# Kernel tuning notes

Hardware: AMD Instinct MI355X
Metric: run time of the kernel (lower is better)

The kernel has to match this reference:

```python
import jax, jax.numpy as jnp
import numpy as np

EPS = 1e-5

def rmsnorm(x, w):
    var = jnp.mean(x * x, axis=-1, keepdims=True)
    return x * jax.lax.rsqrt(var + EPS) * w


def setup_inputs() -> dict:
    key = jax.random.key(0)
    B, L, dim = 4, 2048, 1024
    d_inner, d_state, d_conv, dt_rank = 2 * dim, 16, 4, dim // 16
    ks = jax.random.split(key, 8)
    g = lambda k, shape, scale: (jax.random.normal(k, shape, jnp.float32) * scale)
    return {
        "x": g(ks[0], (B, L, dim), 1.0),
        "rms_w": jnp.ones((dim,), jnp.float32),
        "in_proj": g(ks[1], (dim, 2 * d_inner), dim ** -0.5),
        "conv_w": g(ks[2], (d_inner, d_conv), 0.25),
        "conv_b": jnp.zeros((d_inner,), jnp.float32),
        "x_proj": g(ks[3], (d_inner, dt_rank + 2 * d_state), d_inner ** -0.5),
        "dt_w": g(ks[4], (dt_rank, d_inner), dt_rank ** -0.5),
        # inverse-softplus(0.01): softplus(dt_b) ~ 0.01 at init, standard Mamba dt init
        "dt_b": jnp.full((d_inner,), float(np.log(np.expm1(0.01))), jnp.float32),
        # S4D-real init: A_n = -(n+1)
        "A_log": jnp.log(jnp.broadcast_to(jnp.arange(1, d_state + 1, dtype=jnp.float32), (d_inner, d_state))).copy(),
        "D": jnp.ones((d_inner,), jnp.float32),
        "out_proj": g(ks[5], (d_inner, dim), d_inner ** -0.5),
    }


def _mamba_block(x, rms_w, in_proj, conv_w, conv_b, x_proj, dt_w, dt_b, A_log, D, out_proj):
    B, L, dim = x.shape
    d_inner, K = conv_w.shape
    d_state = A_log.shape[1]
    dt_rank = dt_w.shape[0]

    xn = rmsnorm(x, rms_w)
    xz = xn @ in_proj                      # [B,L,2*d_inner]
    xi, z = jnp.split(xz, 2, axis=-1)

    # causal depthwise conv1d over L
    xc = jax.lax.conv_general_dilated(
        xi.transpose(0, 2, 1),             # [B,C,L]
        conv_w[:, None, :],                # [C,1,K]
        window_strides=(1,), padding=[(K - 1, 0)],
        feature_group_count=d_inner,
    ).transpose(0, 2, 1) + conv_b
    xi = jax.nn.silu(xc)                   # [B,L,d_inner]

    dbc = xi @ x_proj                      # [B,L,dt_rank+2*d_state]
    dt, Bm, Cm = jnp.split(dbc, [dt_rank, dt_rank + d_state], axis=-1)
    delta = jax.nn.softplus(dt @ dt_w + dt_b)  # [B,L,d_inner]
    A = -jnp.exp(A_log)                    # [d_inner,d_state]

    def step(h, inputs):
        d_t, x_t, B_t, C_t = inputs        # [B,d_inner],[B,d_inner],[B,d_state],[B,d_state]
        dA = jnp.exp(d_t[..., None] * A)   # [B,d_inner,d_state]
        h = dA * h + (d_t * x_t)[..., None] * B_t[:, None, :]
        y = jnp.einsum('bds,bs->bd', h, C_t)
        return h, y

    h0 = jnp.zeros((B, d_inner, d_state), x.dtype)
    xs = (delta.transpose(1, 0, 2), xi.transpose(1, 0, 2),
          Bm.transpose(1, 0, 2), Cm.transpose(1, 0, 2))
    _, ys = jax.lax.scan(step, h0, xs)     # ys: [L,B,d_inner]

    y = ys.transpose(1, 0, 2) + xi * D     # D skip connection
    y = y * jax.nn.silu(z)                 # output gate
    return x + y @ out_proj                # residual


def reference(x, rms_w, in_proj, conv_w, conv_b, x_proj, dt_w, dt_b, A_log, D, out_proj):
    return _mamba_block(x, rms_w, in_proj, conv_w, conv_b, x_proj, dt_w, dt_b, A_log, D, out_proj)
```

## Files before the change

kernel.cpp:

```cpp
#include <hip/hip_runtime.h>
#include <hip/hip_bf16.h>
#include <math.h>


#define ROWS 8192
#define DIM 1024
#define DINNER 2048
#define DSTATE 16
#define DTRANK 64
#define LSEQ 2048
#define NCHUNK 32
#define LCHUNK 64

#define LOG2E 1.4426950408889634f

typedef unsigned short ushort;
typedef __attribute__((ext_vector_type(8))) short short8;
typedef __attribute__((ext_vector_type(4))) float float4v;

__device__ inline ushort f2bf(float f) {
    __hip_bfloat16 h = __float2bfloat16(f);
    return *reinterpret_cast<ushort*>(&h);
}
__device__ inline float bf2f(ushort u) {
    union { unsigned int i; float f; } w; w.i = ((unsigned int)u) << 16; return w.f;
}

__device__ inline float fexp2(float x) {
#if __has_builtin(__builtin_amdgcn_exp2f)
    return __builtin_amdgcn_exp2f(x);
#else
    return __expf(x * 0.69314718056f);
#endif
}

__device__ inline void dma16(const void* g, void* l) {
    __builtin_amdgcn_global_load_lds(
        (const __attribute__((address_space(1))) unsigned int*)g,
        (__attribute__((address_space(3))) unsigned int*)l, 16, 0, 0);
}

template <int N> __device__ inline void vwait() {
    if constexpr (N == 0)      asm volatile("s_waitcnt vmcnt(0)" ::: "memory");
    else if constexpr (N == 3) asm volatile("s_waitcnt vmcnt(3)" ::: "memory");
    else if constexpr (N == 4) asm volatile("s_waitcnt vmcnt(4)" ::: "memory");
    else if constexpr (N == 6) asm volatile("s_waitcnt vmcnt(6)" ::: "memory");
    else static_assert(N < 0, "unsupported vmcnt literal");
}

__global__ __launch_bounds__(256)
void prep_kernel(const float* __restrict__ in_proj, ushort* __restrict__ bt1,
                 const float* __restrict__ out_proj, ushort* __restrict__ bt2,
                 const float* __restrict__ x_proj, ushort* __restrict__ bt3,
                 const float* __restrict__ dt_w, ushort* __restrict__ bt4,
                 const float* __restrict__ x, const float* __restrict__ rms_w,
                 ushort* __restrict__ xn) {
    __shared__ float tld[32][33];
    __shared__ float red[4];
    int bid = blockIdx.x, tid = threadIdx.x;
    if (bid < 6464) {
        const float* in; ushort* outT; int R, C, bx, by;
        if (bid < 4096)      { in = in_proj;  outT = bt1; R = 1024; C = 4096; bx = bid & 127; by = bid >> 7; }
        else if (bid < 6144) { int t = bid - 4096; in = out_proj; outT = bt2; R = 2048; C = 1024; bx = t & 31; by = t >> 5; }
        else if (bid < 6336) { int t = bid - 6144; in = x_proj;  outT = bt3; R = 2048; C = 96;  bx = t % 3;  by = t / 3; }
        else                 { int t = bid - 6336; in = dt_w;    outT = bt4; R = 64;   C = 2048; bx = t & 63; by = t >> 6; }
        int tx = tid & 31, ty = tid >> 5;
#pragma unroll
        for (int k = 0; k < 4; ++k)
            tld[ty + k * 8][tx] = in[(long)(by * 32 + ty + k * 8) * C + bx * 32 + tx];
        __syncthreads();
#pragma unroll
        for (int k = 0; k < 4; ++k)
            outT[(long)(bx * 32 + ty + k * 8) * R + by * 32 + tx] = f2bf(tld[tx][ty + k * 8]);
    } else {
        int row = bid - 6464;
        float4 xv = ((const float4*)(x + (long)row * DIM))[tid];
        float ss = xv.x * xv.x + xv.y * xv.y + xv.z * xv.z + xv.w * xv.w;
        for (int off = 32; off > 0; off >>= 1) ss += __shfl_down(ss, off);
        if ((tid & 63) == 0) red[tid >> 6] = ss;
        __syncthreads();
        float scale = rsqrtf((red[0] + red[1] + red[2] + red[3]) / DIM + 1e-5f);
        float4 wv = ((const float4*)rms_w)[tid];
        ushort4 ov;
        ov.x = f2bf(xv.x * scale * wv.x);
        ov.y = f2bf(xv.y * scale * wv.y);
        ov.z = f2bf(xv.z * scale * wv.z);
        ov.w = f2bf(xv.w * scale * wv.w);
        ((ushort4*)xn)[(long)row * 256 + tid] = ov;
    }
}

template <int MW, int NW, int MF, int NF, int EPI>
__global__ __launch_bounds__(MW * NW * 64, 4)
void gemm_ring(const ushort* __restrict__ A, int lda,
               const ushort* __restrict__ Bt, int ldbt,
               void* __restrict__ Cv, int ldc, int K,
               const float* __restrict__ aux) {
    constexpr int W    = MW * NW;
    constexpr int BLKM = MW * MF * 16;
    constexpr int BLKN = NW * NF * 16;
    constexpr int TILE = (BLKM + BLKN) * 32;
    constexpr int NA   = BLKM / (16 * W);
    constexpr int NB   = BLKN / (16 * W);
    __shared__ __align__(16) ushort lds[2 * TILE];

    const int tid  = threadIdx.x;
    const int w    = tid >> 6, lane = tid & 63;
    const int wm   = w / NW,   wn   = w % NW;
    const int quad = lane >> 4, l16 = lane & 15;
    const long row0 = (long)blockIdx.y * BLKM;
    const long col0 = (long)blockIdx.x * BLKN;

    const ushort* gA[NA];
    const ushort* gB[NB];
#pragma unroll
    for (int i = 0; i < NA; ++i)
        gA[i] = A + (row0 + (w + i * W) * 16 + l16) * lda + quad * 8;
#pragma unroll
    for (int i = 0; i < NB; ++i)
        gB[i] = Bt + (col0 + (w + i * W) * 16 + l16) * ldbt + quad * 8;

    const int NT = K >> 5;
    float4v acc[MF][NF] = {};

    auto stage = [&](int kt, int slot) {
        ushort* lb = lds + slot * TILE;
        const int ko = kt << 5;
#pragma unroll
        for (int i = 0; i < NA; ++i)
            dma16(gA[i] + ko, lb + (w + i * W) * 512);
#pragma unroll
        for (int i = 0; i < NB; ++i)
            dma16(gB[i] + ko, lb + BLKM * 32 + (w + i * W) * 512);
    };

    stage(0, 0);
    vwait<0>();
    __builtin_amdgcn_s_barrier();

    for (int t = 0; t < NT; ++t) {
        const int s = t & 1;
        if (t + 1 < NT) stage(t + 1, s ^ 1);
        const ushort* lb  = lds + s * TILE;
        const ushort* lbB = lb + BLKM * 32;
        short8 af[MF], bfr[NF];
#pragma unroll
        for (int m = 0; m < MF; ++m)
            af[m] = *reinterpret_cast<const short8*>(
                &lb[(wm * MF + m) * 512 + lane * 8]);
#pragma unroll
        for (int n = 0; n < NF; ++n)
            bfr[n] = *reinterpret_cast<const short8*>(
                &lbB[(wn * NF + n) * 512 + lane * 8]);
        __builtin_amdgcn_s_setprio(1);
#pragma unroll
        for (int m = 0; m < MF; ++m)
#pragma unroll
            for (int n = 0; n < NF; ++n)
                acc[m][n] = __builtin_amdgcn_mfma_f32_16x16x32_bf16(
                    af[m], bfr[n], acc[m][n], 0, 0, 0);
        __builtin_amdgcn_s_setprio(0);
        vwait<0>();
        if (t < NT - 1) __builtin_amdgcn_s_barrier();
    }

#pragma unroll
    for (int m = 0; m < MF; ++m) {
#pragma unroll
        for (int n = 0; n < NF; ++n) {
            long rbase = row0 + wm * (MF * 16) + m * 16 + quad * 4;
            long c = col0 + wn * (NF * 16) + n * 16 + l16;
#pragma unroll
            for (int r = 0; r < 4; ++r) {
                float v = acc[m][n][r];
                long idx = (rbase + r) * (long)ldc + c;
                if (EPI == 2) ((float*)Cv)[idx] = v + aux[idx];
                else          ((ushort*)Cv)[idx] = f2bf(v);
            }
        }
    }
}

__global__ __launch_bounds__(256)
void xproj_conv_gemm(const ushort* __restrict__ xz,
                     const float* __restrict__ cw, const float* __restrict__ cb,
                     const ushort* __restrict__ bt3,
                     float* __restrict__ dbcp) {
    __shared__ __align__(16) ushort As[128][32];
    __shared__ __align__(16) ushort Bs[128][32];
    int tid = threadIdx.x;
    int wave = tid >> 6, lane = tid & 63;
    int wm = wave >> 1, wn = wave & 1;
    int quad = lane >> 4, l16 = lane & 15;
    int row0 = blockIdx.y * 128;
    int ks0 = blockIdx.x * 512;
    int srow = tid >> 2, sseg = tid & 3;

    int r0 = (wave * 2 + 0) * 16 + (lane >> 2);
    int r1 = (wave * 2 + 1) * 16 + (lane >> 2);
    int ksl = (lane & 3) * 8;
    const ushort* b0 = bt3 + (long)r0 * 2048 + ks0 + ksl;
    const ushort* b1 = bt3 + (long)r1 * 2048 + ks0 + ksl;
    ushort* lB0 = &Bs[(wave * 2 + 0) * 16][0];
    ushort* lB1 = &Bs[(wave * 2 + 1) * 16][0];

    float4v acc[4][4] = {};

    for (int k0 = 0; k0 < 512; k0 += 32) {
        dma16(b0 + k0, lB0);
        dma16(b1 + k0, lB1);
#pragma unroll
        for (int it = 0; it < 2; ++it) {
            int r = srow + it * 64;
            long row = row0 + r;
            int l = (int)(row & (LSEQ - 1));
            int cch = ks0 + k0 + sseg * 8;
            short8 v[4];
#pragma unroll
            for (int t = 0; t < 4; ++t) {
                if (l - 3 + t >= 0) v[t] = *(const short8*)&xz[(row - 3 + t) * 4096 + cch];
                else { short8 zz = {0,0,0,0,0,0,0,0}; v[t] = zz; }
            }
            ushort o[8];
#pragma unroll
            for (int j = 0; j < 8; ++j) {
                float4 w = ((const float4*)cw)[cch + j];
                float a = cb[cch + j]
                        + bf2f((ushort)v[0][j]) * w.x + bf2f((ushort)v[1][j]) * w.y
                        + bf2f((ushort)v[2][j]) * w.z + bf2f((ushort)v[3][j]) * w.w;
                a = a / (1.f + __expf(-a));
                o[j] = f2bf(a);
            }
            *(short8*)&As[r][sseg * 8] = *(const short8*)o;
        }
        __syncthreads();

        short8 afrag[4], bfrag[4];
#pragma unroll
        for (int i = 0; i < 4; ++i)
            afrag[i] = *reinterpret_cast<const short8*>(&As[wm * 64 + i * 16 + l16][quad * 8]);
#pragma unroll
        for (int j = 0; j < 4; ++j)
            bfrag[j] = *reinterpret_cast<const short8*>(&Bs[wn * 64 + j * 16 + l16][quad * 8]);
#pragma unroll
        for (int i = 0; i < 4; ++i)
#pragma unroll
            for (int j = 0; j < 4; ++j)
                acc[i][j] = __builtin_amdgcn_mfma_f32_16x16x32_bf16(
                    afrag[i], bfrag[j], acc[i][j], 0, 0, 0);
        __syncthreads();
    }
    float* dst = dbcp + (long)blockIdx.x * ROWS * 96;
#pragma unroll
    for (int i = 0; i < 4; ++i) {
#pragma unroll
        for (int j = 0; j < 4; ++j) {
            int rbase = row0 + wm * 64 + i * 16 + quad * 4;
            int c = wn * 64 + j * 16 + l16;
            if (c < 96) {
#pragma unroll
                for (int r = 0; r < 4; ++r)
                    dst[(long)(rbase + r) * 96 + c] = acc[i][j][r];
            }
        }
    }
}

__global__ __launch_bounds__(256)
void dbc_reduce(const float4* __restrict__ dbcp, float4* __restrict__ dbc) {
    int i = blockIdx.x * 256 + threadIdx.x;
    float4 a = dbcp[i];
    float4 b = dbcp[i + 196608];
    float4 c = dbcp[i + 2 * 196608];
    float4 d = dbcp[i + 3 * 196608];
    float4 o;
    o.x = a.x + b.x + c.x + d.x;
    o.y = a.y + b.y + c.y + d.y;
    o.z = a.z + b.z + c.z + d.z;
    o.w = a.w + b.w + c.w + d.w;
    dbc[i] = o;
}

__global__ __launch_bounds__(256)
void mfma_gemm_dt(const float* __restrict__ A, int lda,
                  const ushort* __restrict__ Bt, int ldbt,
                  ushort* __restrict__ C, int ldc, int K,
                  const float* __restrict__ aux) {
    __shared__ __align__(16) ushort As[128][40];
    __shared__ __align__(16) ushort Bs[128][40];
    int tid = threadIdx.x;
    int wave = tid >> 6, lane = tid & 63;
    int wm = wave >> 1, wn = wave & 1;
    int quad = lane >> 4, l16 = lane & 15;
    int row0 = blockIdx.y * 128, col0 = blockIdx.x * 128;
    int srow = tid >> 2, sseg = tid & 3;

    float4v acc[4][4] = {};

    for (int k0 = 0; k0 < K; k0 += 32) {
#pragma unroll
        for (int it = 0; it < 2; ++it) {
            int r = srow + it * 64;
            const float* ap = A + (long)(row0 + r) * lda + k0 + sseg * 8;
            ushort tmp[8];
#pragma unroll
            for (int j = 0; j < 8; ++j) tmp[j] = f2bf(ap[j]);
            *reinterpret_cast<short8*>(&As[r][sseg * 8]) =
                *reinterpret_cast<const short8*>(tmp);
            const ushort* bp = Bt + (long)(col0 + r) * ldbt + k0 + sseg * 8;
            *reinterpret_cast<short8*>(&Bs[r][sseg * 8]) =
                *reinterpret_cast<const short8*>(bp);
        }
        __syncthreads();
        short8 afrag[4], bfrag[4];
#pragma unroll
        for (int i = 0; i < 4; ++i)
            afrag[i] = *reinterpret_cast<const short8*>(&As[wm * 64 + i * 16 + l16][quad * 8]);
#pragma unroll
        for (int j = 0; j < 4; ++j)
            bfrag[j] = *reinterpret_cast<const short8*>(&Bs[wn * 64 + j * 16 + l16][quad * 8]);
#pragma unroll
        for (int i = 0; i < 4; ++i)
#pragma unroll
            for (int j = 0; j < 4; ++j)
                acc[i][j] = __builtin_amdgcn_mfma_f32_16x16x32_bf16(
                    afrag[i], bfrag[j], acc[i][j], 0, 0, 0);
        __syncthreads();
    }
#pragma unroll
    for (int i = 0; i < 4; ++i) {
#pragma unroll
        for (int j = 0; j < 4; ++j) {
            int rbase = row0 + wm * 64 + i * 16 + quad * 4;
            int c = col0 + wn * 64 + j * 16 + l16;
#pragma unroll
            for (int r = 0; r < 4; ++r) {
                float v = acc[i][j][r] + aux[c];
                v = (v > 20.f) ? v : __logf(1.f + __expf(v));
                C[(long)(rbase + r) * ldc + c] = f2bf(v);
            }
        }
    }
}

__global__ __launch_bounds__(256)
void scan_part1(const ushort* __restrict__ xz,
                const ushort* __restrict__ dlt,
                const float* __restrict__ dbc,
                const float* __restrict__ A_log,
                const float* __restrict__ cw, const float* __restrict__ cb,
                float* __restrict__ hbuf,
                float* __restrict__ sdbuf) {
    int c = blockIdx.y * 256 + threadIdx.x;
    int b = blockIdx.z, g = blockIdx.x;
    float A2[16];
#pragma unroll
    for (int s = 0; s < 16; ++s) A2[s] = -__expf(A_log[c * 16 + s]) * LOG2E;
    float4 w = ((const float4*)cw)[c];
    float cbc = cb[c];
    float h[16] = {};
    float sumd = 0.f;
    long row0 = (long)b * LSEQ + (long)g * LCHUNK;
    int l0 = g * LCHUNK;
    float x0 = (l0 >= 3) ? bf2f(xz[(row0 - 3) * 4096 + c]) : 0.f;
    float x1 = (l0 >= 2) ? bf2f(xz[(row0 - 2) * 4096 + c]) : 0.f;
    float x2 = (l0 >= 1) ? bf2f(xz[(row0 - 1) * 4096 + c]) : 0.f;
    long row = row0;
    for (int l = 0; l < LCHUNK; ++l, ++row) {
        float x3 = bf2f(xz[row * 4096 + c]);
        float xc = cbc + x0 * w.x + x1 * w.y + x2 * w.z + x3 * w.w;
        xc = xc / (1.f + __expf(-xc));
        x0 = x1; x1 = x2; x2 = x3;
        float d = bf2f(dlt[row * 2048 + c]);
        const float* __restrict__ bc = dbc + row * 96;
        sumd += d;
        float dx = d * xc;
#pragma unroll
        for (int s = 0; s < 16; ++s)
            h[s] = fexp2(d * A2[s]) * h[s] + dx * bc[64 + s];
    }
    long hb = ((long)(b * NCHUNK + g) * 16) * 2048 + c;
#pragma unroll
    for (int s = 0; s < 16; ++s) hbuf[hb + (long)s * 2048] = h[s];
    sdbuf[(long)(b * NCHUNK + g) * 2048 + c] = sumd;
}

__global__ __launch_bounds__(256)
void scan_part2(float* __restrict__ hbuf, const float* __restrict__ sdbuf,
                const float* __restrict__ A_log) {
    int gl = blockIdx.x * 256 + threadIdx.x;
    int c = gl & 2047, s = (gl >> 11) & 15, b = gl >> 15;
    float A2 = -__expf(A_log[c * 16 + s]) * LOG2E;
    float hrun = 0.f;
    for (int g = 0; g < NCHUNK; ++g) {
        long hi = ((long)(b * NCHUNK + g) * 16 + s) * 2048 + c;
        float hout = hbuf[hi];
        float sd = sdbuf[(long)(b * NCHUNK + g) * 2048 + c];
        hbuf[hi] = hrun;
        hrun = fexp2(A2 * sd) * hrun + hout;
    }
}

__global__ __launch_bounds__(256)
void scan_part3(const ushort* __restrict__ xz,
                ushort* __restrict__ dlt,
                const float* __restrict__ dbc,
                const float* __restrict__ A_log,
                const float* __restrict__ cw, const float* __restrict__ cb,
                const float* __restrict__ Dp,
                const float* __restrict__ hbuf) {
    int c = blockIdx.y * 256 + threadIdx.x;
    int b = blockIdx.z, g = blockIdx.x;
    float A2[16], h[16];
#pragma unroll
    for (int s = 0; s < 16; ++s) A2[s] = -__expf(A_log[c * 16 + s]) * LOG2E;
    long hb = ((long)(b * NCHUNK + g) * 16) * 2048 + c;
#pragma unroll
    for (int s = 0; s < 16; ++s) h[s] = hbuf[hb + (long)s * 2048];
    float4 w = ((const float4*)cw)[c];
    float cbc = cb[c];
    float Dc = Dp[c];
    long row0 = (long)b * LSEQ + (long)g * LCHUNK;
    int l0 = g * LCHUNK;
    float x0 = (l0 >= 3) ? bf2f(xz[(row0 - 3) * 4096 + c]) : 0.f;
    float x1 = (l0 >= 2) ? bf2f(xz[(row0 - 2) * 4096 + c]) : 0.f;
    float x2 = (l0 >= 1) ? bf2f(xz[(row0 - 1) * 4096 + c]) : 0.f;
    long row = row0;
    for (int l = 0; l < LCHUNK; ++l, ++row) {
        float x3 = bf2f(xz[row * 4096 + c]);
        float xc = cbc + x0 * w.x + x1 * w.y + x2 * w.z + x3 * w.w;
        xc = xc / (1.f + __expf(-xc));
        x0 = x1; x1 = x2; x2 = x3;
        float d = bf2f(dlt[row * 2048 + c]);
        float z = bf2f(xz[row * 4096 + 2048 + c]);
        const float* __restrict__ bc = dbc + row * 96;
        float dx = d * xc;
        float y = 0.f;
#pragma unroll
        for (int s = 0; s < 16; ++s) {
            h[s] = fexp2(d * A2[s]) * h[s] + dx * bc[64 + s];
            y += h[s] * bc[80 + s];
        }
        float yv = (y + xc * Dc) * (z / (1.f + __expf(-z)));
        dlt[row * 2048 + c] = f2bf(yv);
    }
}

extern "C" void kernel_launch(void* const* d_in, const int* in_sizes, int n_in,
                              void* d_out, int out_size, void* d_ws, size_t ws_size,
                              hipStream_t stream) {
    const float* x        = (const float*)d_in[0];
    const float* rms_w    = (const float*)d_in[1];
    const float* in_proj  = (const float*)d_in[2];
    const float* conv_w   = (const float*)d_in[3];
    const float* conv_b   = (const float*)d_in[4];
    const float* x_proj   = (const float*)d_in[5];
    const float* dt_w     = (const float*)d_in[6];
    const float* dt_b     = (const float*)d_in[7];
    const float* A_log    = (const float*)d_in[8];
    const float* Dp       = (const float*)d_in[9];
    const float* out_proj = (const float*)d_in[10];
    float* out = (float*)d_out;

    char* p = (char*)d_ws;
    ushort* xz  = (ushort*)p;   p += (size_t)ROWS * 4096 * 2;
    ushort* dlt = (ushort*)p;   p += (size_t)ROWS * 2048 * 2;
    float*  dbc = (float*)p;    p += (size_t)ROWS * 96 * 4;
    ushort* bt1 = (ushort*)p;   p += (size_t)4096 * 1024 * 2;
    ushort* bt2 = (ushort*)p;   p += (size_t)1024 * 2048 * 2;
    ushort* bt3 = (ushort*)p;   p += (size_t)128 * 2048 * 2;
    ushort* bt4 = (ushort*)p;   p += (size_t)2048 * 64 * 2;
    ushort* xn  = (ushort*)p;   p += (size_t)ROWS * 1024 * 2;
    float* sdbuf = (float*)p;   p += (size_t)4 * NCHUNK * 2048 * 4;
    float* hbuf  = (float*)xn;
    float* dbcp  = (float*)xn;

    prep_kernel<<<14656, 256, 0, stream>>>(in_proj, bt1, out_proj, bt2,
                                           x_proj, bt3, dt_w, bt4,
                                           x, rms_w, xn);
    gemm_ring<2, 4, 4, 4, 0><<<dim3(4096 / 256, ROWS / 128), 512, 0, stream>>>(
        xn, DIM, bt1, 1024, xz, 4096, DIM, nullptr);
    xproj_conv_gemm<<<dim3(4, ROWS / 128), 256, 0, stream>>>(
        xz, conv_w, conv_b, bt3, dbcp);
    dbc_reduce<<<768, 256, 0, stream>>>((const float4*)dbcp, (float4*)dbc);
    mfma_gemm_dt<<<dim3(2048 / 128, ROWS / 128), 256, 0, stream>>>(
        dbc, 96, bt4, 64, dlt, 2048, DTRANK, dt_b);
    scan_part1<<<dim3(NCHUNK, DINNER / 256, 4), 256, 0, stream>>>(
        xz, dlt, dbc, A_log, conv_w, conv_b, hbuf, sdbuf);
    scan_part2<<<512, 256, 0, stream>>>(hbuf, sdbuf, A_log);
    scan_part3<<<dim3(NCHUNK, DINNER / 256, 4), 256, 0, stream>>>(
        xz, dlt, dbc, A_log, conv_w, conv_b, Dp, hbuf);
    gemm_ring<4, 2, 2, 4, 2><<<dim3(DIM / 128, ROWS / 128), 512, 0, stream>>>(
        dlt, DINNER, bt2, DINNER, out, DIM, DINNER, x);
}
```

Baseline: 509.6 us.

## Deepen GEMM k-step, enlarge tiles, and replace dbc partial reduce with atomics

The ring GEMM now stages 64-wide K slices per buffer, doing two MFMA sub-steps per barrier. The in_proj and out_proj GEMMs use taller 256-row tiles with occupancy lowered to 2 blocks per CU. The x_proj split-K partials are accumulated with atomicAdd into a dbc buffer that prep_kernel zeroes, which removes the separate reduce kernel and the partial buffer traffic. Costs are more LDS and registers per block, fewer resident waves, possible tail imbalance, and atomics that make the summation order nondeterministic.

```diff
diff --git a/kernel.cpp b/kernel.cpp
--- a/kernel.cpp
+++ b/kernel.cpp
@@ -42,9 +42,8 @@
 
 template <int N> __device__ inline void vwait() {
     if constexpr (N == 0)      asm volatile("s_waitcnt vmcnt(0)" ::: "memory");
-    else if constexpr (N == 3) asm volatile("s_waitcnt vmcnt(3)" ::: "memory");
-    else if constexpr (N == 4) asm volatile("s_waitcnt vmcnt(4)" ::: "memory");
     else if constexpr (N == 6) asm volatile("s_waitcnt vmcnt(6)" ::: "memory");
+    else if constexpr (N == 8) asm volatile("s_waitcnt vmcnt(8)" ::: "memory");
     else static_assert(N < 0, "unsupported vmcnt literal");
 }
 
@@ -54,7 +53,7 @@
                  const float* __restrict__ x_proj, ushort* __restrict__ bt3,
                  const float* __restrict__ dt_w, ushort* __restrict__ bt4,
                  const float* __restrict__ x, const float* __restrict__ rms_w,
-                 ushort* __restrict__ xn) {
+                 ushort* __restrict__ xn, float* __restrict__ dbc) {
     __shared__ float tld[32][33];
     __shared__ float red[4];
     int bid = blockIdx.x, tid = threadIdx.x;
@@ -72,7 +71,7 @@
 #pragma unroll
         for (int k = 0; k < 4; ++k)
             outT[(long)(bx * 32 + ty + k * 8) * R + by * 32 + tx] = f2bf(tld[tx][ty + k * 8]);
-    } else {
+    } else if (bid < 14656) {
         int row = bid - 6464;
         float4 xv = ((const float4*)(x + (long)row * DIM))[tid];
         float ss = xv.x * xv.x + xv.y * xv.y + xv.z * xv.z + xv.w * xv.w;
@@ -87,11 +86,15 @@
         ov.z = f2bf(xv.z * scale * wv.z);
         ov.w = f2bf(xv.w * scale * wv.w);
         ((ushort4*)xn)[(long)row * 256 + tid] = ov;
+    } else {
+        int idx = (bid - 14656) * 256 + tid;
+        float4 z = {0.f, 0.f, 0.f, 0.f};
+        ((float4*)dbc)[idx] = z;
     }
 }
 
 template <int MW, int NW, int MF, int NF, int EPI>
-__global__ __launch_bounds__(MW * NW * 64, 4)
+__global__ __launch_bounds__(MW * NW * 64, 2)
 void gemm_ring(const ushort* __restrict__ A, int lda,
                const ushort* __restrict__ Bt, int ldbt,
                void* __restrict__ Cv, int ldc, int K,
@@ -99,7 +102,7 @@
     constexpr int W    = MW * NW;
     constexpr int BLKM = MW * MF * 16;
     constexpr int BLKN = NW * NF * 16;
-    constexpr int TILE = (BLKM + BLKN) * 32;
+    constexpr int TILE = (BLKM + BLKN) * 64;
     constexpr int NA   = BLKM / (16 * W);
     constexpr int NB   = BLKN / (16 * W);
     __shared__ __align__(16) ushort lds[2 * TILE];
@@ -120,18 +123,23 @@
     for (int i = 0; i < NB; ++i)
         gB[i] = Bt + (col0 + (w + i * W) * 16 + l16) * ldbt + quad * 8;
 
-    const int NT = K >> 5;
+    const int NT = K >> 6;
     float4v acc[MF][NF] = {};
 
     auto stage = [&](int kt, int slot) {
-        ushort* lb = lds + slot * TILE;
-        const int ko = kt << 5;
-#pragma unroll
-        for (int i = 0; i < NA; ++i)
-            dma16(gA[i] + ko, lb + (w + i * W) * 512);
-#pragma unroll
-        for (int i = 0; i < NB; ++i)
-            dma16(gB[i] + ko, lb + BLKM * 32 + (w + i * W) * 512);
+        ushort* lb  = lds + slot * TILE;
+        ushort* lbB = lb + BLKM * 64;
+        const int ko = kt << 6;
+#pragma unroll
+        for (int i = 0; i < NA; ++i) {
+            dma16(gA[i] + ko,      lb + ((w + i * W) * 2 + 0) * 512);
+            dma16(gA[i] + ko + 32, lb + ((w + i * W) * 2 + 1) * 512);
+        }
+#pragma unroll
+        for (int i = 0; i < NB; ++i) {
+            dma16(gB[i] + ko,      lbB + ((w + i * W) * 2 + 0) * 512);
+            dma16(gB[i] + ko + 32, lbB + ((w + i * W) * 2 + 1) * 512);
+        }
     };
 
     stage(0, 0);
@@ -142,24 +150,25 @@
         const int s = t & 1;
         if (t + 1 < NT) stage(t + 1, s ^ 1);
         const ushort* lb  = lds + s * TILE;
-        const ushort* lbB = lb + BLKM * 32;
-        short8 af[MF], bfr[NF];
-#pragma unroll
-        for (int m = 0; m < MF; ++m)
-            af[m] = *reinterpret_cast<const short8*>(
-                &lb[(wm * MF + m) * 512 + lane * 8]);
-#pragma unroll
-        for (int n = 0; n < NF; ++n)
-            bfr[n] = *reinterpret_cast<const short8*>(
-                &lbB[(wn * NF + n) * 512 + lane * 8]);
-        __builtin_amdgcn_s_setprio(1);
-#pragma unroll
-        for (int m = 0; m < MF; ++m)
+        const ushort* lbB = lb + BLKM * 64;
+#pragma unroll
+        for (int h = 0; h < 2; ++h) {
+            short8 af[MF], bfr[NF];
+#pragma unroll
+            for (int m = 0; m < MF; ++m)
+                af[m] = *reinterpret_cast<const short8*>(
+                    &lb[((wm * MF + m) * 2 + h) * 512 + lane * 8]);
 #pragma unroll
             for (int n = 0; n < NF; ++n)
-                acc[m][n] = __builtin_amdgcn_mfma_f32_16x16x32_bf16(
-                    af[m], bfr[n], acc[m][n], 0, 0, 0);
-        __builtin_amdgcn_s_setprio(0);
+                bfr[n] = *reinterpret_cast<const short8*>(
+                    &lbB[((wn * NF + n) * 2 + h) * 512 + lane * 8]);
+#pragma unroll
+            for (int m = 0; m < MF; ++m)
+#pragma unroll
+                for (int n = 0; n < NF; ++n)
+                    acc[m][n] = __builtin_amdgcn_mfma_f32_16x16x32_bf16(
+                        af[m], bfr[n], acc[m][n], 0, 0, 0);
+        }
         vwait<0>();
         if (t < NT - 1) __builtin_amdgcn_s_barrier();
     }
@@ -185,7 +194,7 @@
 void xproj_conv_gemm(const ushort* __restrict__ xz,
                      const float* __restrict__ cw, const float* __restrict__ cb,
                      const ushort* __restrict__ bt3,
-                     float* __restrict__ dbcp) {
+                     float* __restrict__ dbc) {
     __shared__ __align__(16) ushort As[128][32];
     __shared__ __align__(16) ushort Bs[128][32];
     int tid = threadIdx.x;
@@ -250,7 +259,6 @@
                     afrag[i], bfrag[j], acc[i][j], 0, 0, 0);
         __syncthreads();
     }
-    float* dst = dbcp + (long)blockIdx.x * ROWS * 96;
 #pragma unroll
     for (int i = 0; i < 4; ++i) {
 #pragma unroll
@@ -260,25 +268,10 @@
             if (c < 96) {
 #pragma unroll
                 for (int r = 0; r < 4; ++r)
-                    dst[(long)(rbase + r) * 96 + c] = acc[i][j][r];
+                    atomicAdd(&dbc[(long)(rbase + r) * 96 + c], acc[i][j][r]);
             }
         }
     }
-}
-
-__global__ __launch_bounds__(256)
-void dbc_reduce(const float4* __restrict__ dbcp, float4* __restrict__ dbc) {
-    int i = blockIdx.x * 256 + threadIdx.x;
-    float4 a = dbcp[i];
-    float4 b = dbcp[i + 196608];
-    float4 c = dbcp[i + 2 * 196608];
-    float4 d = dbcp[i + 3 * 196608];
-    float4 o;
-    o.x = a.x + b.x + c.x + d.x;
-    o.y = a.y + b.y + c.y + d.y;
-    o.z = a.z + b.z + c.z + d.z;
-    o.w = a.w + b.w + c.w + d.w;
-    dbc[i] = o;
 }
 
 __global__ __launch_bounds__(256)
@@ -473,16 +466,14 @@
     ushort* xn  = (ushort*)p;   p += (size_t)ROWS * 1024 * 2;
     float* sdbuf = (float*)p;   p += (size_t)4 * NCHUNK * 2048 * 4;
     float* hbuf  = (float*)xn;
-    float* dbcp  = (float*)xn;
-
-    prep_kernel<<<14656, 256, 0, stream>>>(in_proj, bt1, out_proj, bt2,
+
+    prep_kernel<<<15424, 256, 0, stream>>>(in_proj, bt1, out_proj, bt2,
                                            x_proj, bt3, dt_w, bt4,
-                                           x, rms_w, xn);
-    gemm_ring<2, 4, 4, 4, 0><<<dim3(4096 / 256, ROWS / 128), 512, 0, stream>>>(
+                                           x, rms_w, xn, dbc);
+    gemm_ring<2, 4, 8, 4, 0><<<dim3(4096 / 256, ROWS / 256), 512, 0, stream>>>(
         xn, DIM, bt1, 1024, xz, 4096, DIM, nullptr);
     xproj_conv_gemm<<<dim3(4, ROWS / 128), 256, 0, stream>>>(
-        xz, conv_w, conv_b, bt3, dbcp);
-    dbc_reduce<<<768, 256, 0, stream>>>((const float4*)dbcp, (float4*)dbc);
+        xz, conv_w, conv_b, bt3, dbc);
     mfma_gemm_dt<<<dim3(2048 / 128, ROWS / 128), 256, 0, stream>>>(
         dbc, 96, bt4, 64, dlt, 2048, DTRANK, dt_b);
     scan_part1<<<dim3(NCHUNK, DINNER / 256, 4), 256, 0, stream>>>(
@@ -490,6 +481,6 @@
     scan_part2<<<512, 256, 0, stream>>>(hbuf, sdbuf, A_log);
     scan_part3<<<dim3(NCHUNK, DINNER / 256, 4), 256, 0, stream>>>(
         xz, dlt, dbc, A_log, conv_w, conv_b, Dp, hbuf);
-    gemm_ring<4, 2, 2, 4, 2><<<dim3(DIM / 128, ROWS / 128), 512, 0, stream>>>(
+    gemm_ring<4, 2, 4, 4, 2><<<dim3(DIM / 128, ROWS / 256), 512, 0, stream>>>(
         dlt, DINNER, bt2, DINNER, out, DIM, DINNER, x);
 }
```

New measurement: 501.5 us. Within noise of the previous version (-1.6%).
